# Optimization experiments

Hardware: AMD Instinct MI355X
Metric: run time of the kernel (lower is better)

The kernel has to match this reference:

```python
import jax, jax.numpy as jnp
import numpy as np
from jax import lax

# config (mirrors KeypointExtract init)
NMS_DIST = 4
CONF_THRESH = 0.015
CELL = 8
BORDER = 4
KPT_NUM = 1024
WINDOW_SIZE = 5
TEMP_INIT = 10.0
MAX_CAND = 8192  # fixed candidate budget (top-scoring pixels fed to greedy NMS)


def _make_offsets():
    # linspace(-(ws//2), ws//2, ws//2*2+1) meshgrid -> (R,2) integer offsets (dy, dx)
    lin = np.linspace(-(WINDOW_SIZE // 2), WINDOW_SIZE // 2, num=WINDOW_SIZE // 2 * 2 + 1)
    o0, o1 = np.meshgrid(lin, lin)
    off = np.concatenate([o0.reshape(-1, 1), o1.reshape(-1, 1)], axis=1)
    return jnp.asarray(off.astype(np.int32))  # (R,2)


def depth2space(semi):
    # softmax over 65 channels, drop dustbin, pixel-shuffle 8x8 cells to full res
    dense = jax.nn.softmax(semi, axis=1)
    nodust = dense[:, :-1, :, :]                      # (B,64,Hc,Wc)
    B, C, Hc, Wc = nodust.shape
    cell = CELL
    hm = nodust.transpose(0, 2, 3, 1).reshape(B, Hc, Wc, cell, cell)
    hm = hm.transpose(0, 1, 3, 2, 4).reshape(B, Hc * cell, Wc * cell)
    return hm                                         # (B,H,W)


def greedy_nms(ys, xs, valid, H, W, pad):
    # faithful greedy grid-suppression NMS: candidates arrive sorted by conf desc
    w = 2 * pad + 1
    grid0 = jnp.zeros((H + 2 * pad, W + 2 * pad), dtype=bool)  # True = suppressed

    def step(grid, inp):
        y, x, v = inp
        keep = v & jnp.logical_not(grid[y + pad, x + pad])
        patch = lax.dynamic_slice(grid, (y, x), (w, w))
        grid = lax.dynamic_update_slice(grid, jnp.logical_or(patch, keep), (y, x))
        return grid, keep

    _, kept = lax.scan(step, grid0, (ys, xs, valid))
    return kept


def grid_sample_bilinear(img, gx, gy):
    # torch F.grid_sample, mode=bilinear, padding=zeros, align_corners=False
    B, C, Hc, Wc = img.shape
    ix = (gx + 1.0) * (Wc / 2.0) - 0.5
    iy = (gy + 1.0) * (Hc / 2.0) - 0.5
    x0 = jnp.floor(ix); y0 = jnp.floor(iy)
    wx1 = ix - x0; wy1 = iy - y0
    bidx = jnp.arange(B)[:, None]

    def tap(xi, yi):
        inb = (xi >= 0) & (xi < Wc) & (yi >= 0) & (yi < Hc)
        xc = jnp.clip(xi, 0, Wc - 1).astype(jnp.int32)
        yc = jnp.clip(yi, 0, Hc - 1).astype(jnp.int32)
        v = img[bidx, :, yc, xc]                      # (B,N,C)
        return jnp.where(inb[..., None], v, 0.0)

    v00 = tap(x0, y0); v01 = tap(x0 + 1, y0)
    v10 = tap(x0, y0 + 1); v11 = tap(x0 + 1, y0 + 1)
    w00 = ((1 - wx1) * (1 - wy1))[..., None]
    w01 = (wx1 * (1 - wy1))[..., None]
    w10 = ((1 - wx1) * wy1)[..., None]
    w11 = (wx1 * wy1)[..., None]
    out = v00 * w00 + v01 * w01 + v10 * w10 + v11 * w11  # (B,N,C)
    return out.transpose(0, 2, 1)                        # (B,C,N)


def setup_inputs() -> dict:
    key = jax.random.key(0)
    k1, k2 = jax.random.split(key)
    semi = jax.random.normal(k1, (4, 65, 120, 160), dtype=jnp.float32)
    coarse_desc = jax.random.normal(k2, (4, 256, 120, 160), dtype=jnp.float32)
    temp = jnp.ones((1,), dtype=jnp.float32) * TEMP_INIT
    return {"semi": semi, "coarse_desc": coarse_desc, "temp": temp}


def reference(semi, coarse_desc, temp):
    heatmap = depth2space(semi)                       # (B,H,W)
    B, H, W = heatmap.shape
    offs = _make_offsets()                            # (R,2) = (dy,dx)
    R = offs.shape[0]

    # ---- keypoint detection (no-grad in original) ----
    hm_sg = lax.stop_gradient(heatmap)
    vals, idx = lax.top_k(hm_sg.reshape(B, -1), MAX_CAND)   # sorted conf desc
    ys = (idx // W).astype(jnp.int32)
    xs = (idx % W).astype(jnp.int32)
    valid = vals >= CONF_THRESH
    kept = jax.vmap(lambda y, x, v: greedy_nms(y, x, v, H, W, NMS_DIST))(ys, xs, valid)
    border_ok = (xs >= BORDER) & (xs < W - BORDER) & (ys >= BORDER) & (ys < H - BORDER)
    sel_key = jnp.where(kept & border_ok, vals, -jnp.inf)
    _, sel = lax.top_k(sel_key, KPT_NUM)              # top kpt_num survivors by conf
    ysel = jnp.take_along_axis(ys, sel, axis=1)       # (B,N)
    xsel = jnp.take_along_axis(xs, sel, axis=1)

    # ---- spatial soft-argmax (differentiable) ----
    yy = ysel[:, None, :] + offs[None, :, 0:1]        # (B,R,N)
    xx = xsel[:, None, :] + offs[None, :, 1:2]
    bidx = jnp.arange(B)[:, None, None]
    region = heatmap[bidx, yy, xx]                    # (B,R,N) gather
    attn = jax.nn.softmax(region * temp[0], axis=1)
    offs_f = offs.astype(jnp.float32)
    dy = jnp.einsum('brn,r->bn', attn, offs_f[:, 0])
    dx = jnp.einsum('brn,r->bn', attn, offs_f[:, 1])
    y_f = ysel.astype(jnp.float32) + dy
    x_f = xsel.astype(jnp.float32) + dx
    batch_pts = jnp.stack([x_f, y_f], axis=-1)        # (B,N,2) (x,y)

    # ---- descriptor sampling ----
    gx = x_f / (W / 2.0) - 1.0
    gy = y_f / (H / 2.0) - 1.0
    desc = grid_sample_bilinear(coarse_desc, gx, gy)  # (B,C,N)
    desc = desc / jnp.maximum(jnp.linalg.norm(desc, axis=1, keepdims=True), 1e-12)
    return batch_pts, desc, heatmap
```

## Files before the change

kernel.cpp:

```cpp
#include <hip/hip_runtime.h>
#include <cstdint>

typedef unsigned int u32;
typedef unsigned long long u64;
typedef unsigned short u16;
typedef unsigned char u8;

#define HM_H 960
#define HM_W 1280
#define HM_N (HM_H*HM_W)
#define BATCH 4
#define CAND 8192
#define KPT 1024
#define NCELL 19200

#define WS_HISTA 0x0
#define WS_HISTB 0x100000
#define WS_META  0x200000
#define WS_CAND  0x200400
#define WS_EQ    0x240400
#define WS_SIDX  0x260400
#define WS_SEL   0x280400
#define WS_CM    0x284400
#define WS_CS    0x2CF400
#define WS_SPOT  0x365400
#define WS_BST   0x385400
#define WS_BLST  0x398040
#define WS_CNT   0x3A8040
#define WS_STAT  0x3C8040
#define WS_CLST  0x3D0040
#define WS_CAND2 0x4D0040


__device__ inline double pixval64(const float* __restrict__ semi, const float* __restrict__ cm,
                                  const double* __restrict__ cs, int b, u32 idx){
  u32 y = idx / HM_W, x = idx - y*HM_W;
  u32 hc = y>>3, wc = x>>3, ch = ((y&7)<<3) | (x&7);
  float logit = semi[(((size_t)b*65 + ch)*120 + hc)*160 + wc];
  int cid = b*NCELL + (int)(hc*160 + wc);
  return exp((double)logit - (double)cm[cid]) / cs[cid];
}

__global__ __launch_bounds__(256) void k_heatmap(const float* __restrict__ semi, float* __restrict__ hm,
                          float* __restrict__ cm, double* __restrict__ cs){
  int tid = blockIdx.x*256 + threadIdx.x;
  if (tid >= BATCH*NCELL*8) return;
  int cell = tid >> 3, sub = tid & 7;
  int wc = cell % 160; int hc = (cell/160) % 120; int b = cell / NCELL;
  const float* p = semi + (size_t)b*65*NCELL + hc*160 + wc;
  float r[8];
  #pragma unroll
  for (int i=0;i<8;i++) r[i] = p[(size_t)(sub*8+i)*NCELL];
  float extra = (sub==7) ? p[(size_t)64*NCELL] : -3.0e38f;
  float m = extra;
  #pragma unroll
  for (int i=0;i<8;i++) m = fmaxf(m, r[i]);
  m = fmaxf(m, __shfl_xor(m,1,64));
  m = fmaxf(m, __shfl_xor(m,2,64));
  m = fmaxf(m, __shfl_xor(m,4,64));
  double S = 0.0;
  #pragma unroll
  for (int i=0;i<8;i++) S += exp((double)r[i] - (double)m);
  if (sub==7) S += exp((double)extra - (double)m);
  S += __shfl_xor(S,1,64);
  S += __shfl_xor(S,2,64);
  S += __shfl_xor(S,4,64);
  if (sub==0){ cm[cell]=m; cs[cell]=S; }
  float* out = hm + ((size_t)b*HM_H + hc*8 + sub)*HM_W + wc*8;
  float o[8];
  #pragma unroll
  for (int i=0;i<8;i++) o[i] = (float)(exp((double)r[i] - (double)m) / S);
  *reinterpret_cast<float4*>(out)     = make_float4(o[0],o[1],o[2],o[3]);
  *reinterpret_cast<float4*>(out + 4) = make_float4(o[4],o[5],o[6],o[7]);
}

#define HBIN0 0x3C75u
#define NHBIN 780
__global__ void k_histA(const float* __restrict__ hm, u32* __restrict__ hist){
  __shared__ u32 lh[NHBIN];
  int b = blockIdx.x >> 8;
  int chunk = blockIdx.x & 255;
  for (int i=threadIdx.x;i<NHBIN;i+=256) lh[i]=0;
  __syncthreads();
  const u32 FLOOR = 0x3C75C28Fu;
  const float4* src = (const float4*)(hm + (size_t)b*HM_N);
  int per = (HM_N/4)/256;
  int start = chunk*per;
  for (int i=start+(int)threadIdx.x; i<start+per; i+=256){
    float4 v = src[i];
    u32 bs;
    bs=__float_as_uint(v.x); if (bs>=FLOOR){ u32 bi=(bs>>16)-HBIN0; if(bi>=NHBIN)bi=NHBIN-1; atomicAdd(&lh[bi],1u); }
    bs=__float_as_uint(v.y); if (bs>=FLOOR){ u32 bi=(bs>>16)-HBIN0; if(bi>=NHBIN)bi=NHBIN-1; atomicAdd(&lh[bi],1u); }
    bs=__float_as_uint(v.z); if (bs>=FLOOR){ u32 bi=(bs>>16)-HBIN0; if(bi>=NHBIN)bi=NHBIN-1; atomicAdd(&lh[bi],1u); }
    bs=__float_as_uint(v.w); if (bs>=FLOOR){ u32 bi=(bs>>16)-HBIN0; if(bi>=NHBIN)bi=NHBIN-1; atomicAdd(&lh[bi],1u); }
  }
  __syncthreads();
  u32* h = hist + b*65536 + HBIN0;
  for (int i=threadIdx.x;i<NHBIN;i+=256){
    u32 c=lh[i]; if (c) atomicAdd(&h[i], c);
  }
}

__global__ void k_histB(const float* __restrict__ hm, const u32* __restrict__ meta, u32* __restrict__ hist){
  const u32 FLOOR = 0x3C75C28Fu;
  u32 nv = BATCH*HM_N/4;
  for (u32 i = blockIdx.x*blockDim.x + threadIdx.x; i < nv; i += gridDim.x*blockDim.x){
    float4 v = reinterpret_cast<const float4*>(hm)[i];
    u32 b = (i*4) / HM_N;
    u32 piv = meta[b*64+0];
    u32* h = hist + b*65536;
    u32 bs;
    bs = __float_as_uint(v.x); if (bs >= FLOOR && (bs>>16)==piv) atomicAdd(&h[bs & 0xFFFFu], 1u);
    bs = __float_as_uint(v.y); if (bs >= FLOOR && (bs>>16)==piv) atomicAdd(&h[bs & 0xFFFFu], 1u);
    bs = __float_as_uint(v.z); if (bs >= FLOOR && (bs>>16)==piv) atomicAdd(&h[bs & 0xFFFFu], 1u);
    bs = __float_as_uint(v.w); if (bs >= FLOOR && (bs>>16)==piv) atomicAdd(&h[bs & 0xFFFFu], 1u);
  }
}

__global__ void k_reduce(const u32* __restrict__ hist, u32* __restrict__ meta, int phase){
  int b = blockIdx.x;
  const u32* h = hist + b*65536;
  u32* mb = meta + b*64;
  u32 K = (phase==0) ? (u32)CAND : mb[1];
  int t = threadIdx.x;
  __shared__ u32 suf[1024];
  u32 s = 0;
  for (int i=0;i<64;i++) s += h[t*64+i];
  suf[t]=s; __syncthreads();
  for (int off=1; off<1024; off<<=1){
    u32 add = (t+off<1024) ? suf[t+off] : 0u;
    u32 nv2 = suf[t] + add;
    __syncthreads();
    suf[t]=nv2; __syncthreads();
  }
  u32 total = suf[0];
  u32 cumAbove = (t<1023) ? suf[t+1] : 0u;
  bool found = (cumAbove < K) && (cumAbove + s >= K);
  if (found){
    u32 cum = cumAbove; int bin = 0; u32 cA = cumAbove;
    for (int i=63;i>=0;i--){
      u32 c = h[t*64+i];
      if (cum + c >= K){ bin = t*64+i; cA = cum; break; }
      cum += c;
    }
    if (phase==0){ mb[0]=(u32)bin; mb[2]=cA; mb[1]=K-cA; }
    else {
      u32 V = (mb[0]<<16) | (u32)bin; mb[3]=V;
      u32 cg = mb[2] + cA; mb[4]=cg;
      mb[5] = (cg < (u32)CAND) ? ((u32)CAND - cg) : 0u;
    }
  }
  if (t==0 && total < K){
    if (phase==0){ mb[0]=0; mb[2]=total; mb[1]=K-total; }
    else {
      u32 V = (mb[0]<<16); mb[3]=V;
      u32 cg = mb[2] + total; mb[4]=cg;
      mb[5] = (cg < (u32)CAND) ? ((u32)CAND - cg) : 0u;
    }
  }
}

#define CB_CAP 4800
__global__ __launch_bounds__(256) void k_compact(const float* __restrict__ hm, u32* __restrict__ meta,
                          u64* __restrict__ cand, u32* __restrict__ eq){
  __shared__ u32 pixb[CB_CAP];
  __shared__ u32 bsb[CB_CAP];
  __shared__ u32 eqb[CB_CAP];
  __shared__ u32 cnt, ecnt, gbase, ebase;
  int b = blockIdx.x >> 8;
  int chunk = blockIdx.x & 255;
  if (threadIdx.x==0){ cnt=0u; ecnt=0u; }
  __syncthreads();
  u32 V = meta[b*64+3];
  const float4* src = (const float4*)(hm + (size_t)b*HM_N);
  int per = (HM_N/4)/256;
  int start = chunk*per;
  for (int i=start+(int)threadIdx.x; i<start+per; i+=256){
    float4 v = src[i];
    u32 pix = (u32)i*4u;
    u32 bs4[4];
    bs4[0]=__float_as_uint(v.x); bs4[1]=__float_as_uint(v.y);
    bs4[2]=__float_as_uint(v.z); bs4[3]=__float_as_uint(v.w);
    #pragma unroll
    for (int c2=0;c2<4;c2++){
      u32 bs = bs4[c2];
      if (bs > V){ u32 p = atomicAdd(&cnt,1u); pixb[p]=pix+(u32)c2; bsb[p]=bs; }
      else if (bs == V){ u32 e = atomicAdd(&ecnt,1u); eqb[e]=pix+(u32)c2; }
    }
  }
  __syncthreads();
  if (threadIdx.x==0){
    gbase = cnt  ? atomicAdd(&meta[b*64+6], cnt)  : 0u;
    ebase = ecnt ? atomicAdd(&meta[b*64+7], ecnt) : 0u;
  }
  __syncthreads();
  u32 c0=cnt, e0=ecnt, gb=gbase, eb=ebase;
  for (u32 i=threadIdx.x; i<c0; i+=256){
    u32 s2 = gb+i;
    if (s2 < CAND) cand[(size_t)b*CAND+s2] = (((u64)(~bsb[i]))<<32)|(u64)pixb[i];
  }
  for (u32 i=threadIdx.x; i<e0; i+=256){
    u32 s2 = eb+i;
    if (s2 < CAND) eq[(size_t)b*CAND+s2] = eqb[i];
  }
}

__global__ void k_eqprep(const u32* __restrict__ meta, u64* __restrict__ cand, const u32* __restrict__ eq,
                         const float* __restrict__ semi, const float* __restrict__ cm,
                         const double* __restrict__ cs){
  int b = blockIdx.x;
  __shared__ double vv[64];
  __shared__ u32 ii[64];
  if (threadIdx.x != 0) return;
  const u32* mb = meta + b*64;
  u32 countGt = mb[4], needEq = mb[5], V32 = mb[3];
  int n = (int)mb[7]; if (n > 64) n = 64;
  for (int j=0;j<n;j++){
    ii[j] = eq[(size_t)b*CAND + j];
    vv[j] = pixval64(semi, cm, cs, b, ii[j]);
  }
  for (int j=1;j<n;j++){
    double vj = vv[j]; u32 ij = ii[j];
    int q = j-1;
    while (q >= 0 && (vv[q] < vj || (vv[q] == vj && ii[q] > ij))){
      vv[q+1]=vv[q]; ii[q+1]=ii[q]; q--;
    }
    vv[q+1]=vj; ii[q+1]=ij;
  }
  u64 vq = ((u64)(~V32))<<32;
  for (u32 r=0; r<needEq; r++){
    u64 key = (r < (u32)n) ? (vq | (u64)ii[r]) : ~0ull;
    if (countGt + r < CAND) cand[(size_t)b*CAND + countGt + r] = key;
  }
}

__global__ __launch_bounds__(512,1) void k_sortloc(u64* __restrict__ cand){
  __shared__ u64 sk[2048];
  int blk = blockIdx.x;
  int b = blk >> 2, seg = blk & 3;
  int t = threadIdx.x;
  int lane = t & 63, w = t >> 6;
  int base = w*256 + lane;
  u64* cb = cand + (size_t)b*CAND + seg*2048;
  u64 E[4];
  #pragma unroll
  for (int m=0;m<4;m++) E[m] = cb[base + m*64];

  for (int k2=2; k2<=2048; k2<<=1){
    int j = k2>>1;
    if (j >= 256){
      __syncthreads();
      #pragma unroll
      for (int m=0;m<4;m++) sk[base + m*64] = E[m];
      __syncthreads();
      for (; j>=256; j>>=1){
        int lj = __ffs(j)-1;
        for (int p=t; p<1024; p+=512){
          int i = ((p >> lj) << (lj+1)) | (p & (j-1));
          int l = i | j;
          bool up = ((i & k2)==0);
          u64 a=sk[i], c=sk[l];
          if ((a>c)==up){ sk[i]=c; sk[l]=a; }
        }
        __syncthreads();
      }
      #pragma unroll
      for (int m=0;m<4;m++) E[m] = sk[base + m*64];
      j = 128;
    }
    for (; j>=64; j>>=1){
      int mm = j>>6;
      #pragma unroll
      for (int m=0;m<4;m++){
        if ((m & mm)==0){
          int i = base + m*64;
          bool up = ((i & k2)==0);
          u64 a=E[m], c=E[m|mm];
          if ((a>c)==up){ E[m]=c; E[m|mm]=a; }
        }
      }
    }
    for (; j>=1; j>>=1){
      bool low0 = ((lane & j)==0);
      #pragma unroll
      for (int m=0;m<4;m++){
        int i = base + m*64;
        bool up = ((i & k2)==0);
        bool keepmin = (low0==up);
        u64 P = (u64)__shfl_xor((long long)E[m], j, 64);
        u64 mn = E[m]<P ? E[m] : P;
        u64 mx = E[m]<P ? P : E[m];
        E[m] = keepmin ? mn : mx;
      }
    }
  }
  #pragma unroll
  for (int m=0;m<4;m++) cb[base + m*64] = E[m];
}

__global__ __launch_bounds__(256) void k_merge(const u64* __restrict__ src, u64* __restrict__ dst, int L){
  int tid = blockIdx.x*256 + (int)threadIdx.x;
  if (tid >= BATCH*CAND) return;
  int b = tid >> 13;
  int e = tid & (CAND-1);
  int pairBase = (e / (2*L)) * (2*L);
  int off = e - pairBase;
  const u64* A = src + ((size_t)b<<13) + pairBase;
  const u64* B = A + L;
  bool inA = off < L;
  int i = inA ? off : off - L;
  u64 key = inA ? A[i] : B[i];
  const u64* O = inA ? B : A;
  int lo = 0, hi = L;
  if (inA){
    while (lo < hi){ int mid=(lo+hi)>>1; if (O[mid] < key) lo=mid+1; else hi=mid; }
  } else {
    while (lo < hi){ int mid=(lo+hi)>>1; if (O[mid] <= key) lo=mid+1; else hi=mid; }
  }
  dst[((size_t)b<<13) + pairBase + i + lo] = key;
}

__global__ __launch_bounds__(1024,1) void k_sortfix(const u64* __restrict__ cand, u32* __restrict__ sidx,
                       const float* __restrict__ semi, const float* __restrict__ cm,
                       const double* __restrict__ cs){
  int b = blockIdx.x;
  extern __shared__ u64 sk[];
  int t = threadIdx.x;
  const u64* cb = cand + (size_t)b*CAND;
  for (int i=t;i<CAND;i+=1024) sk[i]=cb[i];
  __syncthreads();
  for (int pass=0; pass<8; pass++){
    int par = pass & 1;
    for (int q=t; q<CAND/2; q+=1024){
      int p = par + 2*q;
      if (p+1 < CAND){
        u64 a = sk[p], c = sk[p+1];
        u32 ha = (u32)(a>>32), hc2 = (u32)(c>>32);
        if (ha == hc2 && ha != 0xFFFFFFFFu){
          double va = pixval64(semi, cm, cs, b, (u32)a);
          double vc = pixval64(semi, cm, cs, b, (u32)c);
          if (va < vc || (va == vc && (u32)a > (u32)c)){ sk[p]=c; sk[p+1]=a; }
        }
      }
    }
    __syncthreads();
  }
  for (int i=t;i<CAND;i+=1024) sidx[(size_t)b*CAND+i] = (u32)sk[i];
}

#define NBX 80
#define NBY 60
#define NBK (NBX*NBY)
#define BSTSTRIDE 4804
__global__ __launch_bounds__(1024) void k_nbuild(const u32* __restrict__ sidx, u32* __restrict__ spot,
                                                 u32* __restrict__ bstG, u16* __restrict__ blistG){
  __shared__ u32 bcnt[NBK];
  __shared__ u32 bst[NBK];
  __shared__ u32 tsum[1024];
  int b = blockIdx.x, t = threadIdx.x;
  const u32* sb = sidx + (size_t)b*CAND;
  for (int i=t;i<NBK;i+=1024) bcnt[i]=0;
  __syncthreads();
  for (int r=t;r<CAND;r+=1024){
    u32 idx = sb[r];
    u32 p;
    if (idx != 0xFFFFFFFFu){
      u32 y = idx/HM_W, x = idx - y*HM_W;
      p = (y<<16)|x;
      atomicAdd(&bcnt[(y>>4)*NBX+(x>>4)], 1u);
    } else p = 0xFFFFFFFFu;
    spot[(size_t)b*CAND+r] = p;
  }
  __syncthreads();
  u32 lsum=0;
  int base5 = t*5;
  if (base5 < NBK){
    #pragma unroll
    for (int j2=0;j2<5;j2++){ int ix=base5+j2; if (ix<NBK) lsum += bcnt[ix]; }
  }
  tsum[t]=lsum;
  __syncthreads();
  for (int off=1; off<1024; off<<=1){
    u32 add = (t>=off)? tsum[t-off] : 0u;
    __syncthreads();
    tsum[t] += add;
    __syncthreads();
  }
  if (base5 < NBK){
    u32 run = (t==0)?0u:tsum[t-1];
    #pragma unroll
    for (int j2=0;j2<5;j2++){
      int ix=base5+j2; if (ix<NBK){ u32 c=bcnt[ix]; bst[ix]=run; run+=c; }
    }
  }
  __syncthreads();
  for (int i=t;i<NBK;i+=1024){ bcnt[i]=bst[i]; bstG[(size_t)b*BSTSTRIDE+i]=bst[i]; }
  if (t==0) bstG[(size_t)b*BSTSTRIDE+NBK] = tsum[1023];
  __syncthreads();
  for (int r=t;r<CAND;r+=1024){
    u32 p = spot[(size_t)b*CAND+r];
    if (p != 0xFFFFFFFFu){
      u32 bu = ((p>>16)>>4)*NBX + ((p&0xFFFFu)>>4);
      u32 slot = atomicAdd(&bcnt[bu],1u);
      blistG[(size_t)b*CAND+slot] = (u16)r;
    }
  }
}

#define CLCAP 12
__global__ __launch_bounds__(256) void k_nconf(const u32* __restrict__ spot, const u32* __restrict__ bstG,
                                               const u16* __restrict__ blistG, u32* __restrict__ cntG,
                                               u8* __restrict__ statG, u16* __restrict__ clistG){
  int b = blockIdx.x >> 5;
  int r = (blockIdx.x & 31)*256 + (int)threadIdx.x;
  const u32* sp = spot + (size_t)b*CAND;
  u32 p = sp[r];
  if (p == 0xFFFFFFFFu){ statG[(size_t)b*CAND+r]=2; return; }
  int y=(int)(p>>16), x=(int)(p&0xFFFFu);
  int by=y>>4, bx=x>>4;
  const u32* bs = bstG + (size_t)b*BSTSTRIDE;
  const u16* bl = blistG + (size_t)b*CAND;
  u16* cl = clistG + ((size_t)b*CAND + r)*CLCAP;
  int cnt=0; bool heavy=false;
  for (int dy=-1; dy<=1; dy++){
    int yy=by+dy; if (yy<0||yy>=NBY) continue;
    for (int dx=-1; dx<=1; dx++){
      int xx=bx+dx; if (xx<0||xx>=NBX) continue;
      int bu=yy*NBX+xx;
      int s=(int)bs[bu], e=(int)bs[bu+1];
      for (int q=s;q<e;q++){
        int j = (int)bl[q];
        if (j >= r) continue;
        u32 pj = sp[j];
        int ady = y-(int)(pj>>16); ady = ady<0?-ady:ady;
        int adx = x-(int)(pj&0xFFFFu); adx = adx<0?-adx:adx;
        if (ady<=4 && adx<=4){
          if (cnt < CLCAP) cl[cnt++] = (u16)j;
          else heavy = true;
        }
      }
    }
  }
  if (heavy){ cntG[(size_t)b*CAND+r]=0xFFFFFFFFu; statG[(size_t)b*CAND+r]=0; }
  else { cntG[(size_t)b*CAND+r]=(u32)cnt; statG[(size_t)b*CAND+r] = (cnt==0)?1:0; }
}

__global__ __launch_bounds__(1024,1) void k_nresolve(const u32* __restrict__ spot, const u32* __restrict__ bstG,
                                                     const u16* __restrict__ blistG, const u32* __restrict__ cntG,
                                                     u8* __restrict__ statG, const u16* __restrict__ clistG,
                                                     u32* __restrict__ sel){
  __shared__ u8 sstat[CAND];
  __shared__ u16 wl[2][CAND];
  __shared__ u32 wcnt[2];
  __shared__ u32 wpass[256];
  __shared__ u32 wpre[256];
  int b = blockIdx.x, t = threadIdx.x;
  const u32* sp = spot + (size_t)b*CAND;
  if (t<2) wcnt[t]=0;
  __syncthreads();
  for (int r=t;r<CAND;r+=1024){
    u8 st = statG[(size_t)b*CAND+r];
    sstat[r]=st;
    if (st==0){ u32 w=atomicAdd(&wcnt[0],1u); wl[0][w]=(u16)r; }
  }
  __syncthreads();
  int cur=0;
  for (int round=0; round<8192; ++round){
    int n = (int)wcnt[cur];
    if (n==0) break;
    int nx = cur^1;
    for (int i=t;i<n;i+=1024){
      int r = (int)wl[cur][i];
      u32 c = cntG[(size_t)b*CAND+r];
      bool supp=false, blocked=false;
      if (c==0xFFFFFFFFu){
        u32 p = sp[r];
        int y=(int)(p>>16), x=(int)(p&0xFFFFu);
        int by=y>>4, bx=x>>4;
        const u32* bs = bstG + (size_t)b*BSTSTRIDE;
        const u16* bl = blistG + (size_t)b*CAND;
        for (int dy=-1; dy<=1 && !supp; dy++){
          int yy=by+dy; if (yy<0||yy>=NBY) continue;
          for (int dx=-1; dx<=1 && !supp; dx++){
            int xx=bx+dx; if (xx<0||xx>=NBX) continue;
            int bu=yy*NBX+xx;
            int s=(int)bs[bu], e=(int)bs[bu+1];
            for (int q=s;q<e;q++){
              int j = (int)bl[q];
              if (j >= r) continue;
              u32 pj = sp[j];
              int ady = y-(int)(pj>>16); ady = ady<0?-ady:ady;
              int adx = x-(int)(pj&0xFFFFu); adx = adx<0?-adx:adx;
              if (ady<=4 && adx<=4){
                u8 st = sstat[j];
                if (st==1){ supp=true; break; }
                if (st==0) blocked=true;
              }
            }
          }
        }
      } else {
        const u16* cl = clistG + ((size_t)b*CAND + r)*CLCAP;
        for (u32 k=0;k<c;k++){
          u8 st = sstat[cl[k]];
          if (st==1){ supp=true; break; }
          if (st==0) blocked=true;
        }
      }
      if (supp) sstat[r]=2;
      else if (!blocked) sstat[r]=1;
      else { u32 w=atomicAdd(&wcnt[nx],1u); wl[nx][w]=(u16)r; }
    }
    __syncthreads();
    if (t==0) wcnt[cur]=0;
    cur = nx;
    __syncthreads();
  }

  if (t < 256){
    u32 w = 0;
    for (int bi2=0;bi2<32;bi2++){
      int r = t*32+bi2;
      if (sstat[r]==1){
        u32 p = sp[r];
        u32 y=p>>16, x=p&0xFFFFu;
        if (x>=4 && x<HM_W-4 && y>=4 && y<HM_H-4) w |= (1u<<bi2);
      }
    }
    wpass[t]=w;
    wpre[t]=__popc(w);
  }
  __syncthreads();
  for (int off=1; off<256; off<<=1){
    u32 add = 0;
    if (t<256 && t>=off) add = wpre[t-off];
    __syncthreads();
    if (t<256) wpre[t] += add;
    __syncthreads();
  }
  u32 P = wpre[255];
  for (int r=t;r<CAND;r+=1024){
    u32 word = wpass[r>>5];
    u32 bit = (u32)r & 31u;
    bool pass = (word>>bit)&1u;
    u32 prank = ((r>>5)>0 ? wpre[(r>>5)-1] : 0u) + __popc(word & ((1u<<bit)-1u));
    u32 p = sp[r];
    u32 y,x;
    if (p==0xFFFFFFFFu){ y=HM_H-1; x=HM_W-1; } else { y=p>>16; x=p&0xFFFFu; }
    if (pass){
      if (prank < KPT) sel[b*KPT+prank] = (y<<16)|x;
    } else {
      u32 frank = (u32)r - prank;
      u32 slot = P + frank;
      if (slot < KPT) sel[b*KPT+slot] = (y<<16)|x;
    }
  }
}

__global__ void k_refine(const u32* __restrict__ sel, const float* __restrict__ hm,
                         const float* __restrict__ temp, float* __restrict__ pts){
  int t = blockIdx.x*256 + threadIdx.x;
  if (t >= BATCH*KPT) return;
  int b = t >> 10;
  u32 p = sel[t];
  int y = (int)(p>>16), x = (int)(p & 0xFFFFu);
  float T = temp[0];
  const float* hb = hm + (size_t)b*HM_N;
  float r[25]; float m = -3.0e38f;
  #pragma unroll
  for (int i=0;i<25;i++){
    int yy = y + (i%5) - 2;
    int xx = x + (i/5) - 2;
    if (yy<0) yy += HM_H; if (yy<0) yy=0; if (yy>HM_H-1) yy=HM_H-1;
    if (xx<0) xx += HM_W; if (xx<0) xx=0; if (xx>HM_W-1) xx=HM_W-1;
    float v = hb[yy*HM_W+xx] * T;
    r[i]=v; m=fmaxf(m,v);
  }
  float s=0.f, dy=0.f, dx=0.f;
  #pragma unroll
  for (int i=0;i<25;i++){
    float e = expf(r[i]-m);
    s += e;
    dy += e * (float)((i%5)-2);
    dx += e * (float)((i/5)-2);
  }
  dy /= s; dx /= s;
  pts[t*2+0] = (float)x + dx;
  pts[t*2+1] = (float)y + dy;
}

__global__ __launch_bounds__(256) void k_desc1(const float* __restrict__ pts, const float* __restrict__ cd,
                                               float* __restrict__ desc){
  extern __shared__ float plane[];
  int blk = blockIdx.x;
  int b = blk >> 8;
  const float4* s4 = (const float4*)(cd + (size_t)blk*NCELL);
  float4* p4 = (float4*)plane;
  for (int i=threadIdx.x; i<NCELL/4; i+=256) p4[i]=s4[i];
  __syncthreads();
  for (int n=threadIdx.x; n<KPT; n+=256){
    float xf = pts[(b*KPT+n)*2+0], yf = pts[(b*KPT+n)*2+1];
    float gx = xf/640.0f - 1.0f;
    float gy = yf/480.0f - 1.0f;
    float ix = (gx+1.0f)*80.0f - 0.5f;
    float iy = (gy+1.0f)*60.0f - 0.5f;
    float x0f = floorf(ix), y0f = floorf(iy);
    float wx1 = ix-x0f, wy1 = iy-y0f;
    int x0=(int)x0f, y0=(int)y0f;
    bool xi0 = (x0>=0)&&(x0<160), xi1 = (x0+1>=0)&&(x0+1<160);
    bool yi0 = (y0>=0)&&(y0<120), yi1 = (y0+1>=0)&&(y0+1<120);
    int xc0 = min(max(x0,0),159),   xc1 = min(max(x0+1,0),159);
    int yc0 = min(max(y0,0),119),   yc1 = min(max(y0+1,0),119);
    float v00 = (xi0&&yi0) ? plane[yc0*160+xc0] : 0.f;
    float v01 = (xi1&&yi0) ? plane[yc0*160+xc1] : 0.f;
    float v10 = (xi0&&yi1) ? plane[yc1*160+xc0] : 0.f;
    float v11 = (xi1&&yi1) ? plane[yc1*160+xc1] : 0.f;
    float out = v00*(1.f-wx1)*(1.f-wy1) + v01*wx1*(1.f-wy1)
              + v10*(1.f-wx1)*wy1      + v11*wx1*wy1;
    desc[(size_t)blk*KPT + n] = out;
  }
}

#define DN_T 32
__global__ __launch_bounds__(256) void k_dnorm(float* __restrict__ desc){
  __shared__ float tile[256*DN_T];
  __shared__ float part[8*DN_T];
  __shared__ float nrm[DN_T];
  int b = blockIdx.x >> 5;
  int n0 = (blockIdx.x & 31)*DN_T;
  int t = threadIdx.x;
  float* db = desc + (size_t)b*256*KPT + n0;
  for (int k=0;k<8;k++){
    int idx = t + 256*k;
    int c = idx >> 3, f4 = idx & 7;
    float4 v = *reinterpret_cast<const float4*>(db + (size_t)c*KPT + f4*4);
    *reinterpret_cast<float4*>(&tile[c*DN_T + f4*4]) = v;
  }
  __syncthreads();
  {
    int n = t & (DN_T-1), q = t >> 5;
    float s = 0.f;
    #pragma unroll
    for (int k=0;k<32;k++){
      float v = tile[(q+8*k)*DN_T + n];
      s += v*v;
    }
    part[q*DN_T + n] = s;
  }
  __syncthreads();
  if (t < DN_T){
    float tot = 0.f;
    #pragma unroll
    for (int q=0;q<8;q++) tot += part[q*DN_T + t];
    nrm[t] = fmaxf(sqrtf(tot), 1e-12f);
  }
  __syncthreads();
  for (int k=0;k<8;k++){
    int idx = t + 256*k;
    int c = idx >> 3, f4 = idx & 7;
    float4 v = *reinterpret_cast<const float4*>(&tile[c*DN_T + f4*4]);
    v.x /= nrm[f4*4+0]; v.y /= nrm[f4*4+1]; v.z /= nrm[f4*4+2]; v.w /= nrm[f4*4+3];
    *reinterpret_cast<float4*>(db + (size_t)c*KPT + f4*4) = v;
  }
}

extern "C" void kernel_launch(void* const* d_in, const int* in_sizes, int n_in,
                              void* d_out, int out_size, void* d_ws, size_t ws_size,
                              hipStream_t stream){
  const float* semi = (const float*)d_in[0];
  const float* cdsc = (const float*)d_in[1];
  const float* temp = (const float*)d_in[2];
  float* pts  = (float*)d_out;
  float* desc = pts + 4*1024*2;
  float* hm   = desc + (size_t)4*256*1024;
  char* ws = (char*)d_ws;
  u32* histA = (u32*)(ws + WS_HISTA);
  u32* histB = (u32*)(ws + WS_HISTB);
  u32* meta  = (u32*)(ws + WS_META);
  u64* cand  = (u64*)(ws + WS_CAND);
  u32* eq    = (u32*)(ws + WS_EQ);
  u32* sidx  = (u32*)(ws + WS_SIDX);
  u32* sel   = (u32*)(ws + WS_SEL);
  float*  cm = (float*)(ws + WS_CM);
  double* cs = (double*)(ws + WS_CS);
  u32* spot  = (u32*)(ws + WS_SPOT);
  u32* bstG  = (u32*)(ws + WS_BST);
  u16* blistG= (u16*)(ws + WS_BLST);
  u32* cntG  = (u32*)(ws + WS_CNT);
  u8*  statG = (u8*)(ws + WS_STAT);
  u16* clistG= (u16*)(ws + WS_CLST);
  u64* cand2 = (u64*)(ws + WS_CAND2);

  hipMemsetAsync(ws, 0, WS_CAND, stream);

  k_heatmap<<<2400, 256, 0, stream>>>(semi, hm, cm, cs);
  k_histA  <<<1024, 256, 0, stream>>>(hm, histA);
  k_reduce <<<4, 1024, 0, stream>>>(histA, meta, 0);
  k_histB  <<<1024, 256, 0, stream>>>(hm, meta, histB);
  k_reduce <<<4, 1024, 0, stream>>>(histB, meta, 1);
  k_compact<<<1024, 256, 0, stream>>>(hm, meta, cand, eq);
  k_eqprep <<<4, 64, 0, stream>>>(meta, cand, eq, semi, cm, cs);
  k_sortloc<<<16, 512, 0, stream>>>(cand);
  k_merge  <<<128, 256, 0, stream>>>(cand, cand2, 2048);
  k_merge  <<<128, 256, 0, stream>>>(cand2, cand, 4096);
  hipFuncSetAttribute((const void*)k_sortfix, hipFuncAttributeMaxDynamicSharedMemorySize, CAND*8);
  k_sortfix<<<4, 1024, CAND*8, stream>>>(cand, sidx, semi, cm, cs);
  k_nbuild <<<4, 1024, 0, stream>>>(sidx, spot, bstG, blistG);
  k_nconf  <<<128, 256, 0, stream>>>(spot, bstG, blistG, cntG, statG, clistG);
  k_nresolve<<<4, 1024, 0, stream>>>(spot, bstG, blistG, cntG, statG, clistG, sel);
  k_refine <<<16, 256, 0, stream>>>(sel, hm, temp, pts);
  hipFuncSetAttribute((const void*)k_desc1, hipFuncAttributeMaxDynamicSharedMemorySize, NCELL*4);
  k_desc1  <<<1024, 256, NCELL*4, stream>>>(pts, cdsc, desc);
  k_dnorm  <<<128, 256, 0, stream>>>(desc);
}
```

Baseline: 200.5 us.

## Fuse coarse histogram into heatmap kernel and merge sortfix with bucket build

The first-pass coarse histogram is now built inside the heatmap softmax kernel from values still in registers, which removes a full extra read of the heatmap and one launch. The bucket-list build for NMS is merged into the sortfix kernel so the sorted indices come straight from shared memory instead of a global sidx buffer, removing another launch and a round trip. k_histB is changed to a chunked per-batch layout that loads the pivot once per block. The fused kernels use more shared memory (the sortfix block now holds both sort keys and bucket arrays), which may limit occupancy, and the heatmap kernel's early-exit guard was removed because the grid exactly covers the work.

```diff
diff --git a/kernel.cpp b/kernel.cpp
--- a/kernel.cpp
+++ b/kernel.cpp
@@ -32,6 +32,9 @@
 #define WS_CAND2 0x4D0040
 
 
+#define HBIN0 0x3C75u
+#define NHBIN 780
+
 __device__ inline double pixval64(const float* __restrict__ semi, const float* __restrict__ cm,
                                   const double* __restrict__ cs, int b, u32 idx){
   u32 y = idx / HM_W, x = idx - y*HM_W;
@@ -42,9 +45,12 @@
 }
 
 __global__ __launch_bounds__(256) void k_heatmap(const float* __restrict__ semi, float* __restrict__ hm,
-                          float* __restrict__ cm, double* __restrict__ cs){
+                          float* __restrict__ cm, double* __restrict__ cs, u32* __restrict__ hist){
+  __shared__ u32 lh[NHBIN];
+  for (int i=threadIdx.x;i<NHBIN;i+=256) lh[i]=0;
+  __syncthreads();
+  const u32 FLOOR = 0x3C75C28Fu;
   int tid = blockIdx.x*256 + threadIdx.x;
-  if (tid >= BATCH*NCELL*8) return;
   int cell = tid >> 3, sub = tid & 7;
   int wc = cell % 160; int hc = (cell/160) % 120; int b = cell / NCELL;
   const float* p = semi + (size_t)b*65*NCELL + hc*160 + wc;
@@ -72,43 +78,30 @@
   for (int i=0;i<8;i++) o[i] = (float)(exp((double)r[i] - (double)m) / S);
   *reinterpret_cast<float4*>(out)     = make_float4(o[0],o[1],o[2],o[3]);
   *reinterpret_cast<float4*>(out + 4) = make_float4(o[4],o[5],o[6],o[7]);
-}
-
-#define HBIN0 0x3C75u
-#define NHBIN 780
-__global__ void k_histA(const float* __restrict__ hm, u32* __restrict__ hist){
-  __shared__ u32 lh[NHBIN];
+  #pragma unroll
+  for (int i=0;i<8;i++){
+    u32 bs = __float_as_uint(o[i]);
+    if (bs>=FLOOR){ u32 bi=(bs>>16)-HBIN0; if(bi>=NHBIN)bi=NHBIN-1; atomicAdd(&lh[bi],1u); }
+  }
+  __syncthreads();
+  u32* h = hist + b*65536 + HBIN0;
+  for (int i=threadIdx.x;i<NHBIN;i+=256){
+    u32 c=lh[i]; if (c) atomicAdd(&h[i], c);
+  }
+}
+
+__global__ __launch_bounds__(256) void k_histB(const float* __restrict__ hm, const u32* __restrict__ meta,
+                                               u32* __restrict__ hist){
+  const u32 FLOOR = 0x3C75C28Fu;
   int b = blockIdx.x >> 8;
   int chunk = blockIdx.x & 255;
-  for (int i=threadIdx.x;i<NHBIN;i+=256) lh[i]=0;
-  __syncthreads();
-  const u32 FLOOR = 0x3C75C28Fu;
+  u32 piv = meta[b*64+0];
+  u32* h = hist + b*65536;
   const float4* src = (const float4*)(hm + (size_t)b*HM_N);
   int per = (HM_N/4)/256;
   int start = chunk*per;
   for (int i=start+(int)threadIdx.x; i<start+per; i+=256){
     float4 v = src[i];
-    u32 bs;
-    bs=__float_as_uint(v.x); if (bs>=FLOOR){ u32 bi=(bs>>16)-HBIN0; if(bi>=NHBIN)bi=NHBIN-1; atomicAdd(&lh[bi],1u); }
-    bs=__float_as_uint(v.y); if (bs>=FLOOR){ u32 bi=(bs>>16)-HBIN0; if(bi>=NHBIN)bi=NHBIN-1; atomicAdd(&lh[bi],1u); }
-    bs=__float_as_uint(v.z); if (bs>=FLOOR){ u32 bi=(bs>>16)-HBIN0; if(bi>=NHBIN)bi=NHBIN-1; atomicAdd(&lh[bi],1u); }
-    bs=__float_as_uint(v.w); if (bs>=FLOOR){ u32 bi=(bs>>16)-HBIN0; if(bi>=NHBIN)bi=NHBIN-1; atomicAdd(&lh[bi],1u); }
-  }
-  __syncthreads();
-  u32* h = hist + b*65536 + HBIN0;
-  for (int i=threadIdx.x;i<NHBIN;i+=256){
-    u32 c=lh[i]; if (c) atomicAdd(&h[i], c);
-  }
-}
-
-__global__ void k_histB(const float* __restrict__ hm, const u32* __restrict__ meta, u32* __restrict__ hist){
-  const u32 FLOOR = 0x3C75C28Fu;
-  u32 nv = BATCH*HM_N/4;
-  for (u32 i = blockIdx.x*blockDim.x + threadIdx.x; i < nv; i += gridDim.x*blockDim.x){
-    float4 v = reinterpret_cast<const float4*>(hm)[i];
-    u32 b = (i*4) / HM_N;
-    u32 piv = meta[b*64+0];
-    u32* h = hist + b*65536;
     u32 bs;
     bs = __float_as_uint(v.x); if (bs >= FLOOR && (bs>>16)==piv) atomicAdd(&h[bs & 0xFFFFu], 1u);
     bs = __float_as_uint(v.y); if (bs >= FLOOR && (bs>>16)==piv) atomicAdd(&h[bs & 0xFFFFu], 1u);
@@ -320,14 +313,22 @@
   dst[((size_t)b<<13) + pairBase + i + lo] = key;
 }
 
-__global__ __launch_bounds__(1024,1) void k_sortfix(const u64* __restrict__ cand, u32* __restrict__ sidx,
+#define NBX 80
+#define NBY 60
+#define NBK (NBX*NBY)
+#define BSTSTRIDE 4804
+__global__ __launch_bounds__(1024,1) void k_sortfix(const u64* __restrict__ cand,
                        const float* __restrict__ semi, const float* __restrict__ cm,
-                       const double* __restrict__ cs){
-  int b = blockIdx.x;
+                       const double* __restrict__ cs,
+                       u32* __restrict__ spot, u32* __restrict__ bstG, u16* __restrict__ blistG){
+  __shared__ u32 bcnt[NBK];
+  __shared__ u32 bst[NBK];
+  __shared__ u32 tsum[1024];
   extern __shared__ u64 sk[];
-  int t = threadIdx.x;
+  int b = blockIdx.x, t = threadIdx.x;
   const u64* cb = cand + (size_t)b*CAND;
   for (int i=t;i<CAND;i+=1024) sk[i]=cb[i];
+  for (int i=t;i<NBK;i+=1024) bcnt[i]=0;
   __syncthreads();
   for (int pass=0; pass<8; pass++){
     int par = pass & 1;
@@ -345,24 +346,8 @@
     }
     __syncthreads();
   }
-  for (int i=t;i<CAND;i+=1024) sidx[(size_t)b*CAND+i] = (u32)sk[i];
-}
-
-#define NBX 80
-#define NBY 60
-#define NBK (NBX*NBY)
-#define BSTSTRIDE 4804
-__global__ __launch_bounds__(1024) void k_nbuild(const u32* __restrict__ sidx, u32* __restrict__ spot,
-                                                 u32* __restrict__ bstG, u16* __restrict__ blistG){
-  __shared__ u32 bcnt[NBK];
-  __shared__ u32 bst[NBK];
-  __shared__ u32 tsum[1024];
-  int b = blockIdx.x, t = threadIdx.x;
-  const u32* sb = sidx + (size_t)b*CAND;
-  for (int i=t;i<NBK;i+=1024) bcnt[i]=0;
-  __syncthreads();
   for (int r=t;r<CAND;r+=1024){
-    u32 idx = sb[r];
+    u32 idx = (u32)sk[r];
     u32 p;
     if (idx != 0xFFFFFFFFu){
       u32 y = idx/HM_W, x = idx - y*HM_W;
@@ -398,9 +383,10 @@
   if (t==0) bstG[(size_t)b*BSTSTRIDE+NBK] = tsum[1023];
   __syncthreads();
   for (int r=t;r<CAND;r+=1024){
-    u32 p = spot[(size_t)b*CAND+r];
-    if (p != 0xFFFFFFFFu){
-      u32 bu = ((p>>16)>>4)*NBX + ((p&0xFFFFu)>>4);
+    u32 idx = (u32)sk[r];
+    if (idx != 0xFFFFFFFFu){
+      u32 y = idx/HM_W, x = idx - y*HM_W;
+      u32 bu = (y>>4)*NBX + (x>>4);
       u32 slot = atomicAdd(&bcnt[bu],1u);
       blistG[(size_t)b*CAND+slot] = (u16)r;
     }
@@ -679,7 +665,6 @@
   u32* meta  = (u32*)(ws + WS_META);
   u64* cand  = (u64*)(ws + WS_CAND);
   u32* eq    = (u32*)(ws + WS_EQ);
-  u32* sidx  = (u32*)(ws + WS_SIDX);
   u32* sel   = (u32*)(ws + WS_SEL);
   float*  cm = (float*)(ws + WS_CM);
   double* cs = (double*)(ws + WS_CS);
@@ -693,8 +678,7 @@
 
   hipMemsetAsync(ws, 0, WS_CAND, stream);
 
-  k_heatmap<<<2400, 256, 0, stream>>>(semi, hm, cm, cs);
-  k_histA  <<<1024, 256, 0, stream>>>(hm, histA);
+  k_heatmap<<<2400, 256, 0, stream>>>(semi, hm, cm, cs, histA);
   k_reduce <<<4, 1024, 0, stream>>>(histA, meta, 0);
   k_histB  <<<1024, 256, 0, stream>>>(hm, meta, histB);
   k_reduce <<<4, 1024, 0, stream>>>(histB, meta, 1);
@@ -704,8 +688,7 @@
   k_merge  <<<128, 256, 0, stream>>>(cand, cand2, 2048);
   k_merge  <<<128, 256, 0, stream>>>(cand2, cand, 4096);
   hipFuncSetAttribute((const void*)k_sortfix, hipFuncAttributeMaxDynamicSharedMemorySize, CAND*8);
-  k_sortfix<<<4, 1024, CAND*8, stream>>>(cand, sidx, semi, cm, cs);
-  k_nbuild <<<4, 1024, 0, stream>>>(sidx, spot, bstG, blistG);
+  k_sortfix<<<4, 1024, CAND*8, stream>>>(cand, semi, cm, cs, spot, bstG, blistG);
   k_nconf  <<<128, 256, 0, stream>>>(spot, bstG, blistG, cntG, statG, clistG);
   k_nresolve<<<4, 1024, 0, stream>>>(spot, bstG, blistG, cntG, statG, clistG, sel);
   k_refine <<<16, 256, 0, stream>>>(sel, hm, temp, pts);
```

Measured after the change: 201.4 us. About the same (+0.4%).
